# Kernel tuning notes

Measured on AMD Instinct MI355X. Metric: run time of the kernel, lower is better.

Reference implementation:

```python
import jax, jax.numpy as jnp
import numpy as np
from jax import lax

H = 2048   # n_hidden
D = 1024   # vect_dim
T = 4096   # timesteps per sequence


def _gru_seq(x, W_ih, W_hh, b_ih, b_hh):
    """Run a GRUCell (PyTorch gate math, gate order r,z,n) over x: [T, D] -> final h [H]."""
    # Precompute all input-to-hidden projections in one batched GEMM: [T, 3H]
    xp = x @ W_ih.T + b_ih

    def step(h, xt):
        hp = h @ W_hh.T + b_hh               # [3H]
        xr, xz, xn = jnp.split(xt, 3)
        hr, hz, hn = jnp.split(hp, 3)
        r = jax.nn.sigmoid(xr + hr)
        z = jax.nn.sigmoid(xz + hz)
        n = jnp.tanh(xn + r * hn)
        h_new = (1.0 - z) * n + z * h
        return h_new, None

    h0 = jnp.zeros((H,), dtype=x.dtype)
    h_final, _ = lax.scan(step, h0, xp)
    return h_final


def setup_inputs() -> dict:
    key = jax.random.key(0)
    ks = jax.random.split(key, 16)
    s_g = 1.0 / np.sqrt(H)   # torch GRUCell init scale
    s_f1 = 1.0 / np.sqrt(2 * H)
    s_f2 = 1.0 / np.sqrt(256)
    return {
        "x1": jax.random.normal(ks[0], (T, D), dtype=jnp.float32),
        "x2": jax.random.normal(ks[1], (T, D), dtype=jnp.float32),
        "W_ih1": jax.random.uniform(ks[2], (3 * H, D), jnp.float32, -s_g, s_g),
        "W_hh1": jax.random.uniform(ks[3], (3 * H, H), jnp.float32, -s_g, s_g),
        "b_ih1": jax.random.uniform(ks[4], (3 * H,), jnp.float32, -s_g, s_g),
        "b_hh1": jax.random.uniform(ks[5], (3 * H,), jnp.float32, -s_g, s_g),
        "W_ih2": jax.random.uniform(ks[6], (3 * H, D), jnp.float32, -s_g, s_g),
        "W_hh2": jax.random.uniform(ks[7], (3 * H, H), jnp.float32, -s_g, s_g),
        "b_ih2": jax.random.uniform(ks[8], (3 * H,), jnp.float32, -s_g, s_g),
        "b_hh2": jax.random.uniform(ks[9], (3 * H,), jnp.float32, -s_g, s_g),
        "fc1_w": jax.random.uniform(ks[10], (256, 2 * H), jnp.float32, -s_f1, s_f1),
        "fc1_b": jax.random.uniform(ks[11], (256,), jnp.float32, -s_f1, s_f1),
        "fc2_w": jax.random.uniform(ks[12], (3, 256), jnp.float32, -s_f2, s_f2),
        "fc2_b": jax.random.uniform(ks[13], (3,), jnp.float32, -s_f2, s_f2),
    }


def reference(x1, x2, W_ih1, W_hh1, b_ih1, b_hh1, W_ih2, W_hh2, b_ih2, b_hh2,
              fc1_w, fc1_b, fc2_w, fc2_b):
    h1 = _gru_seq(x1, W_ih1, W_hh1, b_ih1, b_hh1)   # [H]
    h2 = _gru_seq(x2, W_ih2, W_hh2, b_ih2, b_hh2)   # [H]
    out = jnp.concatenate([h1, h2])[None, :]         # [1, 2H]
    out = jax.nn.relu(out @ fc1_w.T + fc1_b)         # [1, 256]
    out = out @ fc2_w.T + fc2_b                      # [1, 3]
    return jax.nn.log_softmax(out, axis=1)
```

## Files before the change

### kernel.cpp

```cpp
#include <hip/hip_runtime.h>
#include <hip/hip_bf16.h>

constexpr int kH  = 2048;
constexpr int kD  = 1024;
constexpr int kT  = 4096;
constexpr int kTH = 3 * kH;
constexpr int kNB = 256;


__global__ void init_sync_kernel(unsigned* __restrict__ sync) {
    sync[threadIdx.x] = 0u;
}

__global__ __launch_bounds__(256) void gemm_xp_kernel(
    const float* __restrict__ x1, const float* __restrict__ x2,
    const float* __restrict__ Wih1, const float* __restrict__ Wih2,
    const float* __restrict__ bih1, const float* __restrict__ bih2,
    float* __restrict__ xp1, float* __restrict__ xp2) {
    const float* x  = blockIdx.z ? x2   : x1;
    const float* W  = blockIdx.z ? Wih2 : Wih1;
    const float* bi = blockIdx.z ? bih2 : bih1;
    float*       xp = blockIdx.z ? xp2  : xp1;

    __shared__ float As[16][68];
    __shared__ float Bs[16][68];

    const int tid  = threadIdx.x;
    const int tx   = tid & 15, ty = tid >> 4;
    const int lrow = tid >> 2;
    const int lk   = (tid & 3) * 4;
    const int m0   = blockIdx.y * 64;
    const int n0   = blockIdx.x * 64;

    float acc[4][4] = {};

    for (int k0 = 0; k0 < kD; k0 += 16) {
        float4 av = *(const float4*)(x + (size_t)(m0 + lrow) * kD + k0 + lk);
        float4 bv = *(const float4*)(W + (size_t)(n0 + lrow) * kD + k0 + lk);
        __syncthreads();
        As[lk + 0][lrow] = av.x; As[lk + 1][lrow] = av.y;
        As[lk + 2][lrow] = av.z; As[lk + 3][lrow] = av.w;
        Bs[lk + 0][lrow] = bv.x; Bs[lk + 1][lrow] = bv.y;
        Bs[lk + 2][lrow] = bv.z; Bs[lk + 3][lrow] = bv.w;
        __syncthreads();
#pragma unroll
        for (int kk = 0; kk < 16; ++kk) {
            float4 a = *(const float4*)&As[kk][ty * 4];
            float4 b = *(const float4*)&Bs[kk][tx * 4];
            float aa[4] = {a.x, a.y, a.z, a.w};
            float bb[4] = {b.x, b.y, b.z, b.w};
#pragma unroll
            for (int i = 0; i < 4; ++i)
#pragma unroll
                for (int j = 0; j < 4; ++j)
                    acc[i][j] = fmaf(aa[i], bb[j], acc[i][j]);
        }
    }

    float4 bb4 = *(const float4*)(bi + n0 + tx * 4);
    float bArr[4] = {bb4.x, bb4.y, bb4.z, bb4.w};
#pragma unroll
    for (int i = 0; i < 4; ++i) {
        float4 o;
        o.x = acc[i][0] + bArr[0];
        o.y = acc[i][1] + bArr[1];
        o.z = acc[i][2] + bArr[2];
        o.w = acc[i][3] + bArr[3];
        *(float4*)(xp + (size_t)(m0 + ty * 4 + i) * kTH + n0 + tx * 4) = o;
    }
}

__device__ __forceinline__ void grid_barrier_seq(unsigned* __restrict__ base,
                                                 unsigned target, int gid) {
    __syncthreads();
    if (threadIdx.x == 0) {
        unsigned* gcnt = base + gid * 64;
        unsigned* mcnt = base + 4 * 64;
        unsigned* gen  = base + 5 * 64;
        asm volatile("s_waitcnt vmcnt(0)" ::: "memory");
        bool released = false;
        unsigned p = __hip_atomic_fetch_add(gcnt, 1u, __ATOMIC_RELAXED,
                                            __HIP_MEMORY_SCOPE_AGENT);
        if (p == 31u) {
            __hip_atomic_store(gcnt, 0u, __ATOMIC_RELAXED,
                               __HIP_MEMORY_SCOPE_AGENT);
            unsigned q = __hip_atomic_fetch_add(mcnt, 1u, __ATOMIC_RELAXED,
                                                __HIP_MEMORY_SCOPE_AGENT);
            if (q == 3u) {
                __hip_atomic_store(mcnt, 0u, __ATOMIC_RELAXED,
                                   __HIP_MEMORY_SCOPE_AGENT);
                __hip_atomic_fetch_add(gen, 1u, __ATOMIC_RELAXED,
                                       __HIP_MEMORY_SCOPE_AGENT);
                released = true;
            }
        }
        if (!released) {
            while (__hip_atomic_load(gen, __ATOMIC_RELAXED,
                                     __HIP_MEMORY_SCOPE_AGENT) < target) {
                __builtin_amdgcn_s_sleep(1);
            }
        }
    }
    __syncthreads();
}

__global__ __launch_bounds__(512, 2) void gru_pair_kernel(
    const float* __restrict__ xp1, const float* __restrict__ xp2,
    const float* __restrict__ Whh1, const float* __restrict__ Whh2,
    const float* __restrict__ bhh1, const float* __restrict__ bhh2,
    float* __restrict__ h1b0, float* __restrict__ h1b1,
    float* __restrict__ h2b0, float* __restrict__ h2b1,
    unsigned* __restrict__ sync) {
    const int tid  = threadIdx.x;
    const int lane = tid & 63;
    const int wv   = tid >> 6;
    const int b    = blockIdx.x;
    const int s    = b >> 7;
    const int gid  = (b & 127) >> 5;
    const int i0   = (b & 127) * 16;
    const float* xp  = s ? xp2  : xp1;
    const float* Whh = s ? Whh2 : Whh1;
    const float* bhh = s ? bhh2 : bhh1;
    float* hb0 = s ? h2b0 : h1b0;
    float* hb1 = s ? h2b1 : h1b1;
    unsigned* sbase = sync + s * 512;

    __shared__ float h_s[kH];
    __shared__ float hp_s[48];

    float w[6][32];
    float bias[6];
#pragma unroll
    for (int p = 0; p < 6; ++p) {
        const int lr = wv * 6 + p;
        const int g  = lr >> 4, j = lr & 15;
        const int rg = g * kH + i0 + j;
        bias[p] = bhh[rg];
        const float* wr = Whh + (size_t)rg * kH;
#pragma unroll
        for (int e = 0; e < 8; ++e) {
            float4 v = *(const float4*)(wr + e * 256 + lane * 4);
            w[p][e * 4 + 0] = v.x; w[p][e * 4 + 1] = v.y;
            w[p][e * 4 + 2] = v.z; w[p][e * 4 + 3] = v.w;
        }
    }
    {
        const int k = tid * 4;
        *(float4*)&h_s[k] = make_float4(0.f, 0.f, 0.f, 0.f);
    }
    __syncthreads();

    float xr = 0.f, xz = 0.f, xn = 0.f;
    if (tid < 16) {
        const int i = i0 + tid;
        xr = xp[i]; xz = xp[kH + i]; xn = xp[2 * kH + i];
    }

    for (int t = 0; t < kT; ++t) {
        float acc[6];
#pragma unroll
        for (int p = 0; p < 6; ++p) acc[p] = 0.f;
#pragma unroll
        for (int e = 0; e < 8; ++e) {
            const float4 hv = *(const float4*)&h_s[e * 256 + lane * 4];
#pragma unroll
            for (int p = 0; p < 6; ++p) {
                acc[p] = fmaf(w[p][e * 4 + 0], hv.x, acc[p]);
                acc[p] = fmaf(w[p][e * 4 + 1], hv.y, acc[p]);
                acc[p] = fmaf(w[p][e * 4 + 2], hv.z, acc[p]);
                acc[p] = fmaf(w[p][e * 4 + 3], hv.w, acc[p]);
            }
        }
#pragma unroll
        for (int p = 0; p < 6; ++p) {
            float a = acc[p];
#pragma unroll
            for (int off = 32; off; off >>= 1) a += __shfl_down(a, off, 64);
            if (lane == 0) hp_s[wv * 6 + p] = a + bias[p];
        }
        __syncthreads();

        float* dst = ((t + 1) & 1) ? hb1 : hb0;
        float xr_n = 0.f, xz_n = 0.f, xn_n = 0.f;
        if (tid < 16) {
            const int i = i0 + tid;
            const float r = 1.f / (1.f + expf(-(xr + hp_s[tid])));
            const float z = 1.f / (1.f + expf(-(xz + hp_s[16 + tid])));
            const float n = tanhf(xn + r * hp_s[32 + tid]);
            const float hn = (1.f - z) * n + z * h_s[i];
            __hip_atomic_store(&dst[i], hn, __ATOMIC_RELAXED,
                               __HIP_MEMORY_SCOPE_AGENT);
            if (t + 1 < kT) {
                const float* xpt = xp + (size_t)(t + 1) * kTH;
                xr_n = xpt[i]; xz_n = xpt[kH + i]; xn_n = xpt[2 * kH + i];
            }
        }

        grid_barrier_seq(sbase, (unsigned)(t + 1), gid);

        xr = xr_n; xz = xz_n; xn = xn_n;
        {
            const int k = tid * 4;
            unsigned long long lo = __hip_atomic_load(
                (const unsigned long long*)&dst[k], __ATOMIC_RELAXED,
                __HIP_MEMORY_SCOPE_AGENT);
            unsigned long long hi = __hip_atomic_load(
                (const unsigned long long*)&dst[k + 2], __ATOMIC_RELAXED,
                __HIP_MEMORY_SCOPE_AGENT);
            float4 hv;
            hv.x = __uint_as_float((unsigned)(lo & 0xffffffffu));
            hv.y = __uint_as_float((unsigned)(lo >> 32));
            hv.z = __uint_as_float((unsigned)(hi & 0xffffffffu));
            hv.w = __uint_as_float((unsigned)(hi >> 32));
            *(float4*)&h_s[k] = hv;
        }
        __syncthreads();
    }
}

__global__ __launch_bounds__(256) void head_kernel(
    const float* __restrict__ h1, const float* __restrict__ h2,
    const float* __restrict__ fc1w, const float* __restrict__ fc1b,
    const float* __restrict__ fc2w, const float* __restrict__ fc2b,
    float* __restrict__ out) {
    __shared__ float cat[2 * kH];
    __shared__ float o1[256];
    __shared__ float logits[3];
    const int tid  = threadIdx.x;
    const int lane = tid & 63;
    const int wave = tid >> 6;

    for (int k = tid; k < kH; k += 256) {
        cat[k]      = h1[k];
        cat[kH + k] = h2[k];
    }
    __syncthreads();

    for (int r = wave; r < 256; r += 4) {
        const float* wr = fc1w + (size_t)r * (2 * kH);
        float acc = 0.f;
        for (int j = lane; j < 2 * kH; j += 64) acc = fmaf(wr[j], cat[j], acc);
#pragma unroll
        for (int off = 32; off; off >>= 1) acc += __shfl_down(acc, off, 64);
        if (lane == 0) o1[r] = fmaxf(acc + fc1b[r], 0.f);
    }
    __syncthreads();

    if (tid < 3) {
        float acc = fc2b[tid];
        const float* wr = fc2w + tid * 256;
        for (int j = 0; j < 256; ++j) acc = fmaf(wr[j], o1[j], acc);
        logits[tid] = acc;
    }
    __syncthreads();

    if (tid == 0) {
        float m = fmaxf(logits[0], fmaxf(logits[1], logits[2]));
        float s = expf(logits[0] - m) + expf(logits[1] - m) + expf(logits[2] - m);
        float ls = logf(s);
        out[0] = logits[0] - m - ls;
        out[1] = logits[1] - m - ls;
        out[2] = logits[2] - m - ls;
    }
}

extern "C" void kernel_launch(void* const* d_in, const int* in_sizes, int n_in,
                              void* d_out, int out_size, void* d_ws,
                              size_t ws_size, hipStream_t stream) {
    const float* x1   = (const float*)d_in[0];
    const float* x2   = (const float*)d_in[1];
    const float* Wih1 = (const float*)d_in[2];
    const float* Whh1 = (const float*)d_in[3];
    const float* bih1 = (const float*)d_in[4];
    const float* bhh1 = (const float*)d_in[5];
    const float* Wih2 = (const float*)d_in[6];
    const float* Whh2 = (const float*)d_in[7];
    const float* bih2 = (const float*)d_in[8];
    const float* bhh2 = (const float*)d_in[9];
    const float* fc1w = (const float*)d_in[10];
    const float* fc1b = (const float*)d_in[11];
    const float* fc2w = (const float*)d_in[12];
    const float* fc2b = (const float*)d_in[13];
    float* out = (float*)d_out;

    char* ws = (char*)d_ws;
    float* xp1 = (float*)ws;
    float* xp2 = xp1 + (size_t)kT * kTH;
    float* hb  = xp2 + (size_t)kT * kTH;
    float* h1b0 = hb;
    float* h1b1 = hb + kH;
    float* h2b0 = hb + 2 * kH;
    float* h2b1 = hb + 3 * kH;
    unsigned* sync = (unsigned*)(hb + 4 * kH);

    init_sync_kernel<<<1, 1024, 0, stream>>>(sync);

    gemm_xp_kernel<<<dim3(kTH / 64, kT / 64, 2), 256, 0, stream>>>(
        x1, x2, Wih1, Wih2, bih1, bih2, xp1, xp2);

    gru_pair_kernel<<<dim3(kNB), dim3(512), 0, stream>>>(
        xp1, xp2, Whh1, Whh2, bhh1, bhh2, h1b0, h1b1, h2b0, h2b1, sync);

    head_kernel<<<1, 256, 0, stream>>>(h1b0, h2b0, fc1w, fc1b, fc2w, fc2b, out);
}
```

Measured before the change: 21.93 ms.

## Replace hierarchical atomic grid barrier with per-block step flags polled by one wave

Swaps the two-level atomic counter barrier for per-block monotonic step flags. Wave 0 computes the gate update, stores the new h, then publishes its step number. Wave 1 prefetches the next xp slice into double-buffered shared memory and polls all 128 sibling flags with a wave-wide vote. This removes the serialized atomic fetch-add chain and counter resets on each timestep, and takes the xp load off the critical path. In exchange, every block polls 128 flags, which adds load traffic, and the sync buffer grows to four 1024-entry regions.

```diff
diff --git a/kernel.cpp b/kernel.cpp
--- a/kernel.cpp
+++ b/kernel.cpp
@@ -9,7 +9,7 @@
 
 
 __global__ void init_sync_kernel(unsigned* __restrict__ sync) {
-    sync[threadIdx.x] = 0u;
+    sync[blockIdx.x * 1024 + threadIdx.x] = 0u;
 }
 
 __global__ __launch_bounds__(256) void gemm_xp_kernel(
@@ -68,40 +68,6 @@
         o.w = acc[i][3] + bArr[3];
         *(float4*)(xp + (size_t)(m0 + ty * 4 + i) * kTH + n0 + tx * 4) = o;
     }
-}
-
-__device__ __forceinline__ void grid_barrier_seq(unsigned* __restrict__ base,
-                                                 unsigned target, int gid) {
-    __syncthreads();
-    if (threadIdx.x == 0) {
-        unsigned* gcnt = base + gid * 64;
-        unsigned* mcnt = base + 4 * 64;
-        unsigned* gen  = base + 5 * 64;
-        asm volatile("s_waitcnt vmcnt(0)" ::: "memory");
-        bool released = false;
-        unsigned p = __hip_atomic_fetch_add(gcnt, 1u, __ATOMIC_RELAXED,
-                                            __HIP_MEMORY_SCOPE_AGENT);
-        if (p == 31u) {
-            __hip_atomic_store(gcnt, 0u, __ATOMIC_RELAXED,
-                               __HIP_MEMORY_SCOPE_AGENT);
-            unsigned q = __hip_atomic_fetch_add(mcnt, 1u, __ATOMIC_RELAXED,
-                                                __HIP_MEMORY_SCOPE_AGENT);
-            if (q == 3u) {
-                __hip_atomic_store(mcnt, 0u, __ATOMIC_RELAXED,
-                                   __HIP_MEMORY_SCOPE_AGENT);
-                __hip_atomic_fetch_add(gen, 1u, __ATOMIC_RELAXED,
-                                       __HIP_MEMORY_SCOPE_AGENT);
-                released = true;
-            }
-        }
-        if (!released) {
-            while (__hip_atomic_load(gen, __ATOMIC_RELAXED,
-                                     __HIP_MEMORY_SCOPE_AGENT) < target) {
-                __builtin_amdgcn_s_sleep(1);
-            }
-        }
-    }
-    __syncthreads();
 }
 
 __global__ __launch_bounds__(512, 2) void gru_pair_kernel(
@@ -116,17 +82,18 @@
     const int wv   = tid >> 6;
     const int b    = blockIdx.x;
     const int s    = b >> 7;
-    const int gid  = (b & 127) >> 5;
-    const int i0   = (b & 127) * 16;
+    const int lb   = b & 127;
+    const int i0   = lb * 16;
     const float* xp  = s ? xp2  : xp1;
     const float* Whh = s ? Whh2 : Whh1;
     const float* bhh = s ? bhh2 : bhh1;
     float* hb0 = s ? h2b0 : h1b0;
     float* hb1 = s ? h2b1 : h1b1;
-    unsigned* sbase = sync + s * 512;
+    unsigned* flags = sync + s * 2048;
 
     __shared__ float h_s[kH];
     __shared__ float hp_s[48];
+    __shared__ float xp_s[2][48];
 
     float w[6][32];
     float bias[6];
@@ -148,13 +115,10 @@
         const int k = tid * 4;
         *(float4*)&h_s[k] = make_float4(0.f, 0.f, 0.f, 0.f);
     }
-    __syncthreads();
-
-    float xr = 0.f, xz = 0.f, xn = 0.f;
-    if (tid < 16) {
-        const int i = i0 + tid;
-        xr = xp[i]; xz = xp[kH + i]; xn = xp[2 * kH + i];
-    }
+    if (tid < 48) {
+        xp_s[0][tid] = xp[(size_t)(tid >> 4) * kH + i0 + (tid & 15)];
+    }
+    __syncthreads();
 
     for (int t = 0; t < kT; ++t) {
         float acc[6];
@@ -181,24 +145,44 @@
         __syncthreads();
 
         float* dst = ((t + 1) & 1) ? hb1 : hb0;
-        float xr_n = 0.f, xz_n = 0.f, xn_n = 0.f;
-        if (tid < 16) {
-            const int i = i0 + tid;
-            const float r = 1.f / (1.f + expf(-(xr + hp_s[tid])));
-            const float z = 1.f / (1.f + expf(-(xz + hp_s[16 + tid])));
-            const float n = tanhf(xn + r * hp_s[32 + tid]);
-            const float hn = (1.f - z) * n + z * h_s[i];
-            __hip_atomic_store(&dst[i], hn, __ATOMIC_RELAXED,
-                               __HIP_MEMORY_SCOPE_AGENT);
-            if (t + 1 < kT) {
-                const float* xpt = xp + (size_t)(t + 1) * kTH;
-                xr_n = xpt[i]; xz_n = xpt[kH + i]; xn_n = xpt[2 * kH + i];
-            }
-        }
-
-        grid_barrier_seq(sbase, (unsigned)(t + 1), gid);
-
-        xr = xr_n; xz = xz_n; xn = xn_n;
+        if (wv == 0) {
+            if (lane < 16) {
+                const int i = i0 + lane;
+                const float xr = xp_s[t & 1][lane];
+                const float xz = xp_s[t & 1][16 + lane];
+                const float xn = xp_s[t & 1][32 + lane];
+                const float r = 1.f / (1.f + expf(-(xr + hp_s[lane])));
+                const float z = 1.f / (1.f + expf(-(xz + hp_s[16 + lane])));
+                const float n = tanhf(xn + r * hp_s[32 + lane]);
+                const float hn = (1.f - z) * n + z * h_s[i];
+                __hip_atomic_store(&dst[i], hn, __ATOMIC_RELAXED,
+                                   __HIP_MEMORY_SCOPE_AGENT);
+            }
+            asm volatile("s_waitcnt vmcnt(0)" ::: "memory");
+            if (lane == 0) {
+                __hip_atomic_store(&flags[lb * 16], (unsigned)(t + 1),
+                                   __ATOMIC_RELAXED, __HIP_MEMORY_SCOPE_AGENT);
+            }
+        } else if (wv == 1) {
+            if (t + 1 < kT && lane < 48) {
+                xp_s[(t + 1) & 1][lane] =
+                    xp[(size_t)(t + 1) * kTH + (size_t)(lane >> 4) * kH + i0 +
+                       (lane & 15)];
+            }
+            const unsigned tgt = (unsigned)(t + 1);
+            const unsigned* fa = flags + lane * 16;
+            const unsigned* fb = flags + (lane + 64) * 16;
+            for (;;) {
+                unsigned f1 = __hip_atomic_load(fa, __ATOMIC_RELAXED,
+                                                __HIP_MEMORY_SCOPE_AGENT);
+                unsigned f2 = __hip_atomic_load(fb, __ATOMIC_RELAXED,
+                                                __HIP_MEMORY_SCOPE_AGENT);
+                if (__all((f1 >= tgt) && (f2 >= tgt))) break;
+                __builtin_amdgcn_s_sleep(1);
+            }
+        }
+        __syncthreads();
+
         {
             const int k = tid * 4;
             unsigned long long lo = __hip_atomic_load(
@@ -293,7 +277,7 @@
     float* h2b1 = hb + 3 * kH;
     unsigned* sync = (unsigned*)(hb + 4 * kH);
 
-    init_sync_kernel<<<1, 1024, 0, stream>>>(sync);
+    init_sync_kernel<<<4, 1024, 0, stream>>>(sync);
 
     gemm_xp_kernel<<<dim3(kTH / 64, kT / 64, 2), 256, 0, stream>>>(
         x1, x2, Wih1, Wih2, bih1, bih2, xp1, xp2);
```

After: 20.40 ms. 1.07x faster.
